# Kernel tuning notes

Measured on AMD Instinct MI355X. Metric: run time of the kernel, lower is better.

## Reference

```python
import jax, jax.numpy as jnp
import numpy as np

N_NODES = 100000
N_EDGES = 600000
IN_C, HID, OUT_C = 128, 256, 1

def _glorot(key, shape):
    fan_in, fan_out = shape[1], shape[0]
    lim = np.sqrt(6.0 / (fan_in + fan_out))
    return jax.random.uniform(key, shape, jnp.float32, -lim, lim)

def setup_inputs() -> dict:
    key = jax.random.key(0)
    ks = jax.random.split(key, 12)
    x = jax.random.normal(ks[0], (N_NODES, IN_C), jnp.float32)
    edge_index = jax.random.randint(ks[1], (2, N_EDGES), 0, N_NODES, jnp.int32)
    return {
        "x": x,
        "edge_index": edge_index,
        # SAGEConv1: lin_l (neighbors, with bias), lin_r (root, no bias)
        "W1l": _glorot(ks[2], (HID, IN_C)),
        "b1": jnp.zeros((HID,), jnp.float32),
        "W1r": _glorot(ks[3], (HID, IN_C)),
        # SAGEConv2
        "W2l": _glorot(ks[4], (HID, HID)),
        "b2": jnp.zeros((HID,), jnp.float32),
        "W2r": _glorot(ks[5], (HID, HID)),
        # MLP head: Linear(HID, HID//2) -> ReLU -> Linear(HID//2, OUT_C)
        "Wf1": _glorot(ks[6], (HID // 2, HID)),
        "bf1": jnp.zeros((HID // 2,), jnp.float32),
        "Wf2": _glorot(ks[7], (OUT_C, HID // 2)),
        "bf2": jnp.zeros((OUT_C,), jnp.float32),
    }

def _sage_conv(x, src, dst, Wl, b, Wr, n_nodes):
    # mean-aggregate source-node features into destination nodes
    msgs = x[src]  # [E, F] gather
    sums = jax.ops.segment_sum(msgs, dst, num_segments=n_nodes)
    cnt = jax.ops.segment_sum(jnp.ones((src.shape[0], 1), x.dtype), dst,
                              num_segments=n_nodes)
    mean = sums / jnp.maximum(cnt, 1.0)  # isolated nodes -> 0
    return mean @ Wl.T + b + x @ Wr.T

def reference(x, edge_index, W1l, b1, W1r, W2l, b2, W2r, Wf1, bf1, Wf2, bf2):
    src, dst = edge_index[0], edge_index[1]
    n = x.shape[0]
    h = jax.nn.elu(_sage_conv(x, src, dst, W1l, b1, W1r, n))
    # dropout p=0.3 is identity in eval mode
    h = jax.nn.elu(_sage_conv(h, src, dst, W2l, b2, W2r, n))
    h = jax.nn.relu(h @ Wf1.T + bf1)
    out = h @ Wf2.T + bf2  # [N, 1]
    return jnp.squeeze(out)
```

## Files before the change

kernel.cpp:

```cpp
#include <hip/hip_runtime.h>
#include <hip/hip_bf16.h>

#define NN 100000
#define NE 600000
#define NBLK 98
#define MPAD 100096

typedef __attribute__((ext_vector_type(4))) int   i32x4;
typedef __attribute__((ext_vector_type(4))) float f32x4;

__device__ __forceinline__ float b2f(unsigned short u) {
  unsigned int v = ((unsigned int)u) << 16;
  return __uint_as_float(v);
}
__device__ __forceinline__ unsigned short f2b(float f) {
  __hip_bfloat16 h = __float2bfloat16(f);
  return *reinterpret_cast<unsigned short*>(&h);
}
__device__ __forceinline__ float elu(float v) {
  return v > 0.0f ? v : (expf(v) - 1.0f);
}
__device__ __forceinline__ void gload_lds16(const void* g, void* l) {
  __builtin_amdgcn_global_load_lds(
      (const __attribute__((address_space(1))) void*)g,
      (__attribute__((address_space(3))) void*)l, 16, 0, 0);
}
__device__ __forceinline__ f32x4 mfma16(i32x4 a, i32x4 b, f32x4 c) {
  asm volatile("v_mfma_f32_16x16x32_bf16 %0, %1, %2, %0"
               : "+v"(c) : "v"(a), "v"(b));
  return c;
}
#define WAITV(N) asm volatile("s_waitcnt vmcnt(" #N ")" ::: "memory")
#define BAR() asm volatile("s_barrier" ::: "memory")

__global__ __launch_bounds__(256) void hist_kernel(
    const int* __restrict__ ei, int* __restrict__ deg) {
  const int* dst = ei + NE;
  int i = blockIdx.x * 256 + threadIdx.x;
  int n = gridDim.x * 256;
  for (int e = i; e < NE; e += n) atomicAdd(&deg[dst[e]], 1);
}

__global__ __launch_bounds__(256) void scan1_kernel(
    const int* __restrict__ deg, int* __restrict__ row, int* __restrict__ aux) {
  __shared__ int sd[256];
  int b = blockIdx.x, t = threadIdx.x;
  int base = b * 1024 + t * 4;
  int v0 = (base + 0 < NN) ? deg[base + 0] : 0;
  int v1 = (base + 1 < NN) ? deg[base + 1] : 0;
  int v2 = (base + 2 < NN) ? deg[base + 2] : 0;
  int v3 = (base + 3 < NN) ? deg[base + 3] : 0;
  int s = v0 + v1 + v2 + v3;
  sd[t] = s;
  __syncthreads();
  for (int off = 1; off < 256; off <<= 1) {
    int tmp = (t >= off) ? sd[t - off] : 0;
    __syncthreads();
    sd[t] += tmp;
    __syncthreads();
  }
  int excl = sd[t] - s;
  if (base + 0 < NN) row[base + 0] = excl;
  if (base + 1 < NN) row[base + 1] = excl + v0;
  if (base + 2 < NN) row[base + 2] = excl + v0 + v1;
  if (base + 3 < NN) row[base + 3] = excl + v0 + v1 + v2;
  if (t == 255) aux[b] = sd[t];
}

__global__ __launch_bounds__(256) void scan2_kernel(int* __restrict__ aux) {
  __shared__ int sd[256];
  int t = threadIdx.x;
  int v = (t < NBLK) ? aux[t] : 0;
  sd[t] = v;
  __syncthreads();
  for (int off = 1; off < 256; off <<= 1) {
    int tmp = (t >= off) ? sd[t - off] : 0;
    __syncthreads();
    sd[t] += tmp;
    __syncthreads();
  }
  if (t < NBLK) aux[t] = sd[t] - v;
}

__global__ __launch_bounds__(256) void scan3_kernel(
    int* __restrict__ row, const int* __restrict__ aux) {
  int i = blockIdx.x * 256 + threadIdx.x;
  if (i < NN) row[i] += aux[i >> 10];
  if (i == 0) row[NN] = NE;
}

__global__ __launch_bounds__(256) void fill_kernel(
    const int* __restrict__ ei, const int* __restrict__ row,
    int* __restrict__ cur, int* __restrict__ eidx) {
  const int* src = ei;
  const int* dst = ei + NE;
  int i = blockIdx.x * 256 + threadIdx.x;
  int n = gridDim.x * 256;
  for (int e = i; e < NE; e += n) {
    int d = dst[e];
    int p = atomicAdd(&cur[d], 1);
    eidx[row[d] + p] = src[e];
  }
}

__global__ __launch_bounds__(256) void conv_x(
    const float* __restrict__ x, unsigned short* __restrict__ A1) {
  int i = blockIdx.x * 256 + threadIdx.x;
  if (i >= NN * 32) return;
  int n = i >> 5, k4 = i & 31;
  float4 v = ((const float4*)(x + (size_t)n * 128))[k4];
  ushort4 o;
  o.x = f2b(v.x); o.y = f2b(v.y); o.z = f2b(v.z); o.w = f2b(v.w);
  ((ushort4*)(A1 + (size_t)n * 256 + 128))[k4] = o;
}

__global__ __launch_bounds__(256) void conv_w(
    const float* __restrict__ W1l, const float* __restrict__ W1r,
    const float* __restrict__ W2l, const float* __restrict__ W2r,
    const float* __restrict__ Wf1,
    unsigned short* __restrict__ W1b, unsigned short* __restrict__ W2b,
    unsigned short* __restrict__ Wf1b) {
  int i = blockIdx.x * 256 + threadIdx.x;
  const float* srcp;
  unsigned short* dstp;
  if (i < 16384) {
    int e = i * 4, j = e >> 8, k = e & 255;
    srcp = (k < 128) ? (W1l + (size_t)j * 128 + k) : (W1r + (size_t)j * 128 + (k - 128));
    dstp = W1b + e;
  } else if (i < 49152) {
    int e = (i - 16384) * 4, j = e >> 9, k = e & 511;
    srcp = (k < 256) ? (W2l + (size_t)j * 256 + k) : (W2r + (size_t)j * 256 + (k - 256));
    dstp = W2b + e;
  } else if (i < 57344) {
    int e = (i - 49152) * 4;
    srcp = Wf1 + e;
    dstp = Wf1b + e;
  } else return;
  float4 v = *(const float4*)srcp;
  ushort4 o;
  o.x = f2b(v.x); o.y = f2b(v.y); o.z = f2b(v.z); o.w = f2b(v.w);
  *(ushort4*)dstp = o;
}

__global__ __launch_bounds__(256) void agg1_csr(
    unsigned short* __restrict__ A1, const int* __restrict__ row,
    const int* __restrict__ eidx) {
  int lane = threadIdx.x & 63;
  int n = (blockIdx.x * 256 + threadIdx.x) >> 6;
  if (n >= NN) return;
  int r0 = row[n], r1 = row[n + 1];
  float ax = 0.f, ay = 0.f;
  int e = r0;
  for (; e + 3 < r1; e += 4) {
    int s0 = eidx[e], s1 = eidx[e + 1], s2 = eidx[e + 2], s3 = eidx[e + 3];
    ushort2 a = ((const ushort2*)(A1 + (size_t)s0 * 256 + 128))[lane];
    ushort2 b = ((const ushort2*)(A1 + (size_t)s1 * 256 + 128))[lane];
    ushort2 c = ((const ushort2*)(A1 + (size_t)s2 * 256 + 128))[lane];
    ushort2 d = ((const ushort2*)(A1 + (size_t)s3 * 256 + 128))[lane];
    ax += (b2f(a.x) + b2f(b.x)) + (b2f(c.x) + b2f(d.x));
    ay += (b2f(a.y) + b2f(b.y)) + (b2f(c.y) + b2f(d.y));
  }
  for (; e < r1; ++e) {
    int s0 = eidx[e];
    ushort2 a = ((const ushort2*)(A1 + (size_t)s0 * 256 + 128))[lane];
    ax += b2f(a.x);
    ay += b2f(a.y);
  }
  float inv = 1.0f / (float)max(r1 - r0, 1);
  ushort2 o;
  o.x = f2b(ax * inv);
  o.y = f2b(ay * inv);
  ((ushort2*)(A1 + (size_t)n * 256))[lane] = o;
}

__global__ __launch_bounds__(256) void agg2_csr(
    unsigned short* __restrict__ A2, const int* __restrict__ row,
    const int* __restrict__ eidx) {
  int lane = threadIdx.x & 63;
  int n = (blockIdx.x * 256 + threadIdx.x) >> 6;
  if (n >= NN) return;
  int r0 = row[n], r1 = row[n + 1];
  float4 acc = make_float4(0.f, 0.f, 0.f, 0.f);
  int e = r0;
  for (; e + 3 < r1; e += 4) {
    int s0 = eidx[e], s1 = eidx[e + 1], s2 = eidx[e + 2], s3 = eidx[e + 3];
    ushort4 a = ((const ushort4*)(A2 + (size_t)s0 * 512 + 256))[lane];
    ushort4 b = ((const ushort4*)(A2 + (size_t)s1 * 512 + 256))[lane];
    ushort4 c = ((const ushort4*)(A2 + (size_t)s2 * 512 + 256))[lane];
    ushort4 d = ((const ushort4*)(A2 + (size_t)s3 * 512 + 256))[lane];
    acc.x += (b2f(a.x) + b2f(b.x)) + (b2f(c.x) + b2f(d.x));
    acc.y += (b2f(a.y) + b2f(b.y)) + (b2f(c.y) + b2f(d.y));
    acc.z += (b2f(a.z) + b2f(b.z)) + (b2f(c.z) + b2f(d.z));
    acc.w += (b2f(a.w) + b2f(b.w)) + (b2f(c.w) + b2f(d.w));
  }
  for (; e < r1; ++e) {
    int s0 = eidx[e];
    ushort4 a = ((const ushort4*)(A2 + (size_t)s0 * 512 + 256))[lane];
    acc.x += b2f(a.x);
    acc.y += b2f(a.y);
    acc.z += b2f(a.z);
    acc.w += b2f(a.w);
  }
  float inv = 1.0f / (float)max(r1 - r0, 1);
  ushort4 o;
  o.x = f2b(acc.x * inv);
  o.y = f2b(acc.y * inv);
  o.z = f2b(acc.z * inv);
  o.w = f2b(acc.w * inv);
  ((ushort4*)(A2 + (size_t)n * 512))[lane] = o;
}

template <int K, int APITCH, int EPI>
__global__ __launch_bounds__(256, 3) void gemm_kernel(
    const unsigned short* __restrict__ A, const unsigned short* __restrict__ Wb,
    const float* __restrict__ bias, const float* __restrict__ w2,
    const float* __restrict__ bf2p,
    unsigned short* __restrict__ Hout, int HPITCH, int HOFF,
    float* __restrict__ out) {
  __shared__ unsigned short lA[3][4096];
  __shared__ unsigned short lB[3][4096];
  int tid = threadIdx.x;
  int w = tid >> 6, lane = tid & 63;
  int lhi = lane >> 4, llo = lane & 15;
  int m0 = blockIdx.x * 128;
  int c0 = blockIdx.y * 128;
  int fb = lane * 8;

  f32x4 acc0[8], acc1[8];
#pragma unroll
  for (int n = 0; n < 8; ++n) { acc0[n] = (f32x4)0.f; acc1[n] = (f32x4)0.f; }

#define STAGE(t)                                                                \
  do {                                                                          \
    int _b = (t) % 3;                                                           \
    int _k0 = (t) * 32;                                                         \
    _Pragma("unroll")                                                           \
    for (int i = 0; i < 2; ++i) {                                               \
      int c = w * 2 + i;                                                        \
      const unsigned short* ga =                                                \
          A + (size_t)(m0 + c * 16 + llo) * APITCH + _k0 + lhi * 8;             \
      gload_lds16(ga, &lA[_b][c * 512]);                                        \
      const unsigned short* gb =                                                \
          Wb + (size_t)(c0 + c * 16 + llo) * K + _k0 + lhi * 8;                 \
      gload_lds16(gb, &lB[_b][c * 512]);                                        \
    }                                                                           \
  } while (0)

  constexpr int NSTEP = K / 32;
  STAGE(0);
  STAGE(1);
  for (int t = 0; t < NSTEP; ++t) {
    if (t + 2 < NSTEP) {
      STAGE(t + 2);
      WAITV(8);
    } else if (t + 1 < NSTEP) {
      WAITV(4);
    } else {
      WAITV(0);
    }
    BAR();
    const unsigned short* la = &lA[t % 3][0];
    const unsigned short* lb = &lB[t % 3][0];
    i32x4 a0 = *(const i32x4*)(la + (w * 2 + 0) * 512 + fb);
    i32x4 a1 = *(const i32x4*)(la + (w * 2 + 1) * 512 + fb);
#pragma unroll
    for (int n = 0; n < 8; ++n) {
      i32x4 b = *(const i32x4*)(lb + n * 512 + fb);
      acc0[n] = mfma16(a0, b, acc0[n]);
      acc1[n] = mfma16(a1, b, acc1[n]);
    }
    BAR();
  }
#undef STAGE
  asm volatile("s_nop 7\n\ts_nop 7");

  if constexpr (EPI == 0) {
    float bv[8];
#pragma unroll
    for (int n = 0; n < 8; ++n) bv[n] = bias[c0 + n * 16 + llo];
#pragma unroll
    for (int mi = 0; mi < 2; ++mi) {
#pragma unroll
      for (int n = 0; n < 8; ++n) {
        f32x4 av = mi ? acc1[n] : acc0[n];
#pragma unroll
        for (int r = 0; r < 4; ++r) {
          int R = m0 + (w * 2 + mi) * 16 + lhi * 4 + r;
          float v = elu(av[r] + bv[n]);
          Hout[(size_t)R * HPITCH + HOFF + c0 + n * 16 + llo] = f2b(v);
        }
      }
    }
  } else {
    float b1v[8], w2v[8];
#pragma unroll
    for (int n = 0; n < 8; ++n) {
      b1v[n] = bias[n * 16 + llo];
      w2v[n] = w2[n * 16 + llo];
    }
    float bf2v = bf2p[0];
#pragma unroll
    for (int mi = 0; mi < 2; ++mi) {
#pragma unroll
      for (int r = 0; r < 4; ++r) {
        float s = 0.f;
#pragma unroll
        for (int n = 0; n < 8; ++n) {
          f32x4 av = mi ? acc1[n] : acc0[n];
          s += fmaxf(av[r] + b1v[n], 0.f) * w2v[n];
        }
        s += __shfl_xor(s, 1);
        s += __shfl_xor(s, 2);
        s += __shfl_xor(s, 4);
        s += __shfl_xor(s, 8);
        int R = m0 + (w * 2 + mi) * 16 + lhi * 4 + r;
        if (llo == 0 && R < NN) out[R] = s + bf2v;
      }
    }
  }
}

extern "C" void kernel_launch(void* const* d_in, const int* in_sizes, int n_in,
                              void* d_out, int out_size, void* d_ws, size_t ws_size,
                              hipStream_t stream) {
  const float* x   = (const float*)d_in[0];
  const int*   ei  = (const int*)d_in[1];
  const float* W1l = (const float*)d_in[2];
  const float* b1  = (const float*)d_in[3];
  const float* W1r = (const float*)d_in[4];
  const float* W2l = (const float*)d_in[5];
  const float* b2  = (const float*)d_in[6];
  const float* W2r = (const float*)d_in[7];
  const float* Wf1 = (const float*)d_in[8];
  const float* bf1 = (const float*)d_in[9];
  const float* Wf2 = (const float*)d_in[10];
  const float* bf2 = (const float*)d_in[11];
  float* out = (float*)d_out;

  char* ws = (char*)d_ws;
  size_t o = 0;
  int* deg = (int*)(ws + o); o += 400384;
  int* cur = (int*)(ws + o); o += 400384;
  size_t zero_bytes = o;
  int* row  = (int*)(ws + o); o += 400640;
  int* aux  = (int*)(ws + o); o += 4096;
  int* eidx = (int*)(ws + o); o += 2400000;
  unsigned short* A1 = (unsigned short*)(ws + o); o += (size_t)MPAD * 256 * 2;
  unsigned short* A2 = (unsigned short*)(ws + o); o += (size_t)MPAD * 512 * 2;
  unsigned short* h2 = (unsigned short*)(ws + o); o += (size_t)MPAD * 256 * 2;
  unsigned short* W1b  = (unsigned short*)(ws + o); o += 131072;
  unsigned short* W2b  = (unsigned short*)(ws + o); o += 262144;
  unsigned short* Wf1b = (unsigned short*)(ws + o); o += 65536;

  hipMemsetAsync(d_ws, 0, zero_bytes, stream);

  hist_kernel<<<2048, 256, 0, stream>>>(ei, deg);
  scan1_kernel<<<NBLK, 256, 0, stream>>>(deg, row, aux);
  scan2_kernel<<<1, 256, 0, stream>>>(aux);
  scan3_kernel<<<(NN + 255) / 256, 256, 0, stream>>>(row, aux);
  fill_kernel<<<2048, 256, 0, stream>>>(ei, row, cur, eidx);

  conv_x<<<(NN * 32 + 255) / 256, 256, 0, stream>>>(x, A1);
  conv_w<<<224, 256, 0, stream>>>(W1l, W1r, W2l, W2r, Wf1, W1b, W2b, Wf1b);

  agg1_csr<<<25000, 256, 0, stream>>>(A1, row, eidx);
  gemm_kernel<256, 256, 0><<<dim3(MPAD / 128, 2), 256, 0, stream>>>(
      A1, W1b, b1, nullptr, nullptr, A2, 512, 256, nullptr);
  agg2_csr<<<25000, 256, 0, stream>>>(A2, row, eidx);
  gemm_kernel<512, 512, 0><<<dim3(MPAD / 128, 2), 256, 0, stream>>>(
      A2, W2b, b2, nullptr, nullptr, h2, 256, 0, nullptr);
  gemm_kernel<256, 256, 1><<<dim3(MPAD / 128, 1), 256, 0, stream>>>(
      h2, Wf1b, bf1, Wf2, bf2, nullptr, 0, 0, out);
}
```

Measured before the change: 319.7 us.

## Widen GEMM tile to full output width and switch to double-buffered pipeline

The two SAGE GEMMs now compute all 256 output columns per block (NF=16) instead of splitting columns across blockIdx.y, so each A tile is loaded once rather than twice. The LDS pipeline drops from triple buffering with partial vmcnt waits to double buffering with a full wait and a single barrier per step, issuing the next stage after the barrier. Accumulator count doubles, which raises register pressure, and launch bounds are lowered to 2 blocks per CU. Load latency is hidden less well because each step waits for all outstanding loads.

```diff
diff --git a/kernel.cpp b/kernel.cpp
--- a/kernel.cpp
+++ b/kernel.cpp
@@ -30,7 +30,7 @@
                : "+v"(c) : "v"(a), "v"(b));
   return c;
 }
-#define WAITV(N) asm volatile("s_waitcnt vmcnt(" #N ")" ::: "memory")
+#define WAITV0() asm volatile("s_waitcnt vmcnt(0)" ::: "memory")
 #define BAR() asm volatile("s_barrier" ::: "memory")
 
 __global__ __launch_bounds__(256) void hist_kernel(
@@ -210,29 +210,28 @@
   ((ushort4*)(A2 + (size_t)n * 512))[lane] = o;
 }
 
-template <int K, int APITCH, int EPI>
-__global__ __launch_bounds__(256, 3) void gemm_kernel(
+template <int K, int APITCH, int NF, int EPI>
+__global__ __launch_bounds__(256, 2) void gemm_kernel(
     const unsigned short* __restrict__ A, const unsigned short* __restrict__ Wb,
     const float* __restrict__ bias, const float* __restrict__ w2,
     const float* __restrict__ bf2p,
     unsigned short* __restrict__ Hout, int HPITCH, int HOFF,
     float* __restrict__ out) {
-  __shared__ unsigned short lA[3][4096];
-  __shared__ unsigned short lB[3][4096];
+  __shared__ unsigned short lA[2][4096];
+  __shared__ unsigned short lB[2][NF * 512];
   int tid = threadIdx.x;
   int w = tid >> 6, lane = tid & 63;
   int lhi = lane >> 4, llo = lane & 15;
   int m0 = blockIdx.x * 128;
-  int c0 = blockIdx.y * 128;
   int fb = lane * 8;
 
-  f32x4 acc0[8], acc1[8];
-#pragma unroll
-  for (int n = 0; n < 8; ++n) { acc0[n] = (f32x4)0.f; acc1[n] = (f32x4)0.f; }
+  f32x4 acc0[NF], acc1[NF];
+#pragma unroll
+  for (int n = 0; n < NF; ++n) { acc0[n] = (f32x4)0.f; acc1[n] = (f32x4)0.f; }
 
 #define STAGE(t)                                                                \
   do {                                                                          \
-    int _b = (t) % 3;                                                           \
+    int _b = (t) & 1;                                                           \
     int _k0 = (t) * 32;                                                         \
     _Pragma("unroll")                                                           \
     for (int i = 0; i < 2; ++i) {                                               \
@@ -240,61 +239,57 @@
       const unsigned short* ga =                                                \
           A + (size_t)(m0 + c * 16 + llo) * APITCH + _k0 + lhi * 8;             \
       gload_lds16(ga, &lA[_b][c * 512]);                                        \
+    }                                                                           \
+    _Pragma("unroll")                                                           \
+    for (int i = 0; i < NF / 4; ++i) {                                          \
+      int c = w * (NF / 4) + i;                                                 \
       const unsigned short* gb =                                                \
-          Wb + (size_t)(c0 + c * 16 + llo) * K + _k0 + lhi * 8;                 \
+          Wb + (size_t)(c * 16 + llo) * K + _k0 + lhi * 8;                      \
       gload_lds16(gb, &lB[_b][c * 512]);                                        \
     }                                                                           \
   } while (0)
 
   constexpr int NSTEP = K / 32;
   STAGE(0);
-  STAGE(1);
   for (int t = 0; t < NSTEP; ++t) {
-    if (t + 2 < NSTEP) {
-      STAGE(t + 2);
-      WAITV(8);
-    } else if (t + 1 < NSTEP) {
-      WAITV(4);
-    } else {
-      WAITV(0);
-    }
+    WAITV0();
     BAR();
-    const unsigned short* la = &lA[t % 3][0];
-    const unsigned short* lb = &lB[t % 3][0];
+    if (t + 1 < NSTEP) STAGE(t + 1);
+    const unsigned short* la = &lA[t & 1][0];
+    const unsigned short* lb = &lB[t & 1][0];
     i32x4 a0 = *(const i32x4*)(la + (w * 2 + 0) * 512 + fb);
     i32x4 a1 = *(const i32x4*)(la + (w * 2 + 1) * 512 + fb);
 #pragma unroll
-    for (int n = 0; n < 8; ++n) {
+    for (int n = 0; n < NF; ++n) {
       i32x4 b = *(const i32x4*)(lb + n * 512 + fb);
       acc0[n] = mfma16(a0, b, acc0[n]);
       acc1[n] = mfma16(a1, b, acc1[n]);
     }
-    BAR();
   }
 #undef STAGE
   asm volatile("s_nop 7\n\ts_nop 7");
 
   if constexpr (EPI == 0) {
-    float bv[8];
-#pragma unroll
-    for (int n = 0; n < 8; ++n) bv[n] = bias[c0 + n * 16 + llo];
+    float bv[NF];
+#pragma unroll
+    for (int n = 0; n < NF; ++n) bv[n] = bias[n * 16 + llo];
 #pragma unroll
     for (int mi = 0; mi < 2; ++mi) {
 #pragma unroll
-      for (int n = 0; n < 8; ++n) {
+      for (int n = 0; n < NF; ++n) {
         f32x4 av = mi ? acc1[n] : acc0[n];
 #pragma unroll
         for (int r = 0; r < 4; ++r) {
           int R = m0 + (w * 2 + mi) * 16 + lhi * 4 + r;
           float v = elu(av[r] + bv[n]);
-          Hout[(size_t)R * HPITCH + HOFF + c0 + n * 16 + llo] = f2b(v);
+          Hout[(size_t)R * HPITCH + HOFF + n * 16 + llo] = f2b(v);
         }
       }
     }
   } else {
-    float b1v[8], w2v[8];
-#pragma unroll
-    for (int n = 0; n < 8; ++n) {
+    float b1v[NF], w2v[NF];
+#pragma unroll
+    for (int n = 0; n < NF; ++n) {
       b1v[n] = bias[n * 16 + llo];
       w2v[n] = w2[n * 16 + llo];
     }
@@ -305,7 +300,7 @@
       for (int r = 0; r < 4; ++r) {
         float s = 0.f;
 #pragma unroll
-        for (int n = 0; n < 8; ++n) {
+        for (int n = 0; n < NF; ++n) {
           f32x4 av = mi ? acc1[n] : acc0[n];
           s += fmaxf(av[r] + b1v[n], 0.f) * w2v[n];
         }
@@ -364,11 +359,11 @@
   conv_w<<<224, 256, 0, stream>>>(W1l, W1r, W2l, W2r, Wf1, W1b, W2b, Wf1b);
 
   agg1_csr<<<25000, 256, 0, stream>>>(A1, row, eidx);
-  gemm_kernel<256, 256, 0><<<dim3(MPAD / 128, 2), 256, 0, stream>>>(
+  gemm_kernel<256, 256, 16, 0><<<MPAD / 128, 256, 0, stream>>>(
       A1, W1b, b1, nullptr, nullptr, A2, 512, 256, nullptr);
   agg2_csr<<<25000, 256, 0, stream>>>(A2, row, eidx);
-  gemm_kernel<512, 512, 0><<<dim3(MPAD / 128, 2), 256, 0, stream>>>(
+  gemm_kernel<512, 512, 16, 0><<<MPAD / 128, 256, 0, stream>>>(
       A2, W2b, b2, nullptr, nullptr, h2, 256, 0, nullptr);
-  gemm_kernel<256, 256, 1><<<dim3(MPAD / 128, 1), 256, 0, stream>>>(
+  gemm_kernel<256, 256, 8, 1><<<MPAD / 128, 256, 0, stream>>>(
       h2, Wf1b, bf1, Wf2, bf2, nullptr, 0, 0, out);
 }
```

Measured after the change: 327.1 us. +2.3%, slower.
